# Performance work log

Hardware: AMD Instinct MI355X
Metric: run time of the kernel (lower is better)

The kernel has to match this reference:

```python
import jax, jax.numpy as jnp
import numpy as np

NEG = -1e9
EPS = 1e-5


def _layernorm(x, g, b):
    m = x.mean(-1, keepdims=True)
    v = ((x - m) ** 2).mean(-1, keepdims=True)
    return (x - m) / jnp.sqrt(v + EPS) * g + b


def _layer(h_aug, H_inc, mask_neg, W1, W1_hat, ctx1, W2, W2_hat, W3, g, b):
    # h_aug: (T, H), H_inc/mask_neg: (T, E)
    H = h_aug.shape[-1]
    scale = 1.0 / jnp.sqrt(jnp.asarray(H, h_aug.dtype))
    # Stage 1: node -> hyperedge attention
    proj_hat = h_aug @ W1_hat.T                       # (T, H)
    raw = (proj_hat * ctx1).sum(-1) * scale           # (T,)
    score = raw[:, None] + mask_neg                   # (T, E)
    alpha = jax.nn.softmax(score, axis=0) * H_inc     # (T, E)
    hyper = alpha.T @ (h_aug @ W1.T)                  # (E, H)
    # Stage 2: hyperedge -> node attention
    proj2_hat = hyper @ W2_hat.T                      # (E, H)
    score_ne = (h_aug @ W3.T) @ proj2_hat.T * scale + mask_neg  # (T, E)
    beta = jax.nn.softmax(score_ne, axis=1) * H_inc   # (T, E)
    out = beta @ (hyper @ W2.T)                       # (T, H)
    return _layernorm(out + h_aug, g, b)


def reference(node_emb, H_inc, membership, W1, W1_hat, ctx1, W2, W2_hat, W3, ln_g, ln_b, region_init):
    B, N, H = node_emb.shape
    R = region_init.shape[0]
    L = W1.shape[0]
    mask_neg = jnp.where(H_inc == 0, NEG, 0.0).astype(node_emb.dtype)
    counts = jax.ops.segment_sum(jnp.ones((N,), node_emb.dtype), membership, num_segments=R)
    safe_counts = jnp.maximum(counts, 1.0)

    def per_sample(h):  # h: (N, H)
        sums = jax.ops.segment_sum(h, membership, num_segments=R)     # (R, H)
        reg = jnp.where(counts[:, None] > 0, sums / safe_counts[:, None], 0.0)
        reg = reg + region_init
        h_aug = jnp.concatenate([h, reg], axis=0)                     # (N+R, H)
        for l in range(L):
            h_aug = _layer(h_aug, H_inc, mask_neg, W1[l], W1_hat[l], ctx1[l],
                           W2[l], W2_hat[l], W3[l], ln_g[l], ln_b[l])
        return h_aug[:N]

    return jax.vmap(per_sample)(node_emb)


def setup_inputs() -> dict:
    key = jax.random.key(0)
    ks = jax.random.split(key, 12)
    B, N, R, E, H, L = 4, 8000, 16, 1024, 128, 2
    T = N + R
    w_std = 1.0 / np.sqrt(H)
    node_emb = jax.random.normal(ks[0], (B, N, H), dtype=jnp.float32)
    H_inc = (jax.random.uniform(ks[1], (T, E)) < 0.05).astype(jnp.float32)
    membership = jax.random.randint(ks[2], (N,), 0, R, dtype=jnp.int32)
    W1 = jax.random.normal(ks[3], (L, H, H), dtype=jnp.float32) * w_std
    W1_hat = jax.random.normal(ks[4], (L, H, H), dtype=jnp.float32) * w_std
    ctx1 = jax.random.normal(ks[5], (L, H), dtype=jnp.float32) * 0.02
    W2 = jax.random.normal(ks[6], (L, H, H), dtype=jnp.float32) * w_std
    W2_hat = jax.random.normal(ks[7], (L, H, H), dtype=jnp.float32) * w_std
    W3 = jax.random.normal(ks[8], (L, H, H), dtype=jnp.float32) * w_std
    ln_g = jnp.ones((L, H), dtype=jnp.float32)
    ln_b = jnp.zeros((L, H), dtype=jnp.float32)
    region_init = jax.random.normal(ks[9], (R, H), dtype=jnp.float32) * 0.02
    return {"node_emb": node_emb, "H_inc": H_inc, "membership": membership,
            "W1": W1, "W1_hat": W1_hat, "ctx1": ctx1, "W2": W2, "W2_hat": W2_hat,
            "W3": W3, "ln_g": ln_g, "ln_b": ln_b, "region_init": region_init}
```

## Files before the change

kernel.cpp:

```cpp
#include <hip/hip_runtime.h>

#define HD 128
#define CAPE 768
#define MAXR 16
#define NB_RS 128
#define KSTR 136
#define VSTR 72
#define PSTR 72

typedef unsigned short u16;
typedef unsigned long long u64;
typedef __attribute__((ext_vector_type(8))) short bf16x8;
typedef __attribute__((ext_vector_type(4))) float f32x4;

__device__ inline float b2f(unsigned u){ return __uint_as_float(u << 16); }
__device__ inline u16 f2b(float x){
  unsigned u = __float_as_uint(x);
  return (u16)((u + 0x7fffu + ((u >> 16) & 1u)) >> 16);
}

__device__ inline float waveSum(float v){ for(int o=32;o;o>>=1) v += __shfl_down(v,o); return v; }
__device__ inline float waveMax(float v){ for(int o=32;o;o>>=1) v = fmaxf(v,__shfl_down(v,o)); return v; }

__device__ inline float blockSum128(float v, float* red){
  int j = threadIdx.x;
  float s = waveSum(v);
  __syncthreads();
  if ((j & 63) == 0) red[j >> 6] = s;
  __syncthreads();
  return red[0] + red[1];
}
__device__ inline float blockMax128(float v, float* red){
  int j = threadIdx.x;
  float s = waveMax(v);
  __syncthreads();
  if ((j & 63) == 0) red[j >> 6] = s;
  __syncthreads();
  return fmaxf(red[0], red[1]);
}

__global__ void k_count(const int* __restrict__ memb, int N, int* __restrict__ counts){
  __shared__ int h[64];
  int tid = threadIdx.x;
  if (tid < 64) h[tid] = 0;
  __syncthreads();
  for (int t = blockIdx.x*blockDim.x + tid; t < N; t += gridDim.x*blockDim.x)
    atomicAdd(&h[memb[t]], 1);
  __syncthreads();
  if (tid < 64){ int v = h[tid]; if (v) atomicAdd(&counts[tid], v); }
}

__global__ __launch_bounds__(128) void k_regsum_fast(const float* __restrict__ node,
                        const int* __restrict__ memb, int N, int R,
                        float* __restrict__ partials){
  int b = blockIdx.y, j = threadIdx.x, blk = blockIdx.x;
  int nb = gridDim.x;
  int per = (N + nb - 1) / nb;
  int t0 = blk * per;
  int t1 = t0 + per; if (t1 > N) t1 = N;
  float acc[MAXR];
  #pragma unroll
  for (int i = 0; i < MAXR; ++i) acc[i] = 0.f;
  const float* base = node + (long)b*N*HD + j;
  for (int t = t0; t < t1; ++t){
    float v = base[(long)t*HD];
    int r = memb[t];
    #pragma unroll
    for (int i = 0; i < MAXR; ++i) acc[i] += (i == r) ? v : 0.f;
  }
  float* dst = partials + ((long)(b*nb + blk)*R)*HD + j;
  #pragma unroll
  for (int i = 0; i < MAXR; ++i)
    if (i < R) dst[(long)i*HD] = acc[i];
}

__global__ void k_regsum_lds(const float* __restrict__ node, const int* __restrict__ memb,
                             int N, int R, float* __restrict__ partials, int nb){
  extern __shared__ float acc[];
  int b = blockIdx.y, j = threadIdx.x;
  for (int r = 0; r < R; ++r) acc[r*HD + j] = 0.f;
  int per = (N + gridDim.x - 1) / gridDim.x;
  int t0 = blockIdx.x * per;
  int t1 = t0 + per; if (t1 > N) t1 = N;
  for (int t = t0; t < t1; ++t){
    int r = memb[t];
    acc[r*HD + j] += node[((long)b*N + t)*HD + j];
  }
  for (int r = 0; r < R; ++r)
    atomicAdd(&partials[((long)(b*nb)*R + r)*HD + j], acc[r*HD + j]);
}

__global__ void k_regfin(const float* __restrict__ partials, int nb, int redN,
                         const int* __restrict__ counts,
                         const float* __restrict__ rinit, float* __restrict__ h_aug,
                         int N, int R, int T, int B){
  int i = blockIdx.x*blockDim.x + threadIdx.x;
  if (i >= B*R*HD) return;
  int j = i % HD; int r = (i/HD) % R; int b = i/(HD*R);
  float s = 0.f;
  for (int blk = 0; blk < redN; ++blk)
    s += partials[((long)(b*nb + blk)*R + r)*HD + j];
  int c = counts[r];
  float v = (c > 0) ? s / (float)c : 0.f;
  v += rinit[r*HD + j];
  h_aug[((long)b*T + N + r)*HD + j] = v;
}

__global__ __launch_bounds__(128) void k_copyraw(const float* __restrict__ node,
                      const float* __restrict__ v, float* __restrict__ h_aug,
                      float* __restrict__ raw, int N, int T, float scale){
  int t = blockIdx.x, b = blockIdx.y, j = threadIdx.x;
  __shared__ float red[2];
  long rowb = (long)b*T + t;
  float x;
  if (t < N){ x = node[((long)b*N + t)*HD + j]; h_aug[rowb*HD + j] = x; }
  else      { x = h_aug[rowb*HD + j]; }
  float s = blockSum128(x * v[j], red);
  if (j == 0) raw[rowb] = s * scale;
}

__global__ __launch_bounds__(256) void k_maskbuild(const float* __restrict__ Hinc, int E, int MW,
                        u64* __restrict__ maskw){
  int t = blockIdx.x;
  int wv = threadIdx.x >> 6, lane = threadIdx.x & 63;
  const float* hrow = Hinc + (long)t*E;
  for (int w = wv; w < MW; w += 4){
    int e = w*64 + lane;
    bool f = (e < E) && (hrow[e] != 0.f);
    u64 mk = __ballot(f);
    if (lane == 0) maskw[(long)t*MW + w] = mk;
  }
}

__global__ __launch_bounds__(256) void k_colbuild2(const u64* __restrict__ maskw, int T, int MW,
                           u16* __restrict__ colidx, int* __restrict__ colcnt){
  int e = blockIdx.x;
  int w = e >> 6, bit = e & 63;
  int j = threadIdx.x;
  int lane = j & 63, wv = j >> 6;
  __shared__ int wsum[4];
  int c = 0;
  for (int base = 0; base < T; base += 256){
    int t = base + j;
    bool f = (t < T) && ((maskw[(long)t*MW + w] >> bit) & 1ull);
    u64 mk = __ballot(f);
    if (lane == 0) wsum[wv] = __popcll(mk);
    __syncthreads();
    int pre = 0;
    #pragma unroll
    for (int k = 0; k < 4; ++k) pre += (k < wv) ? wsum[k] : 0;
    int tot = wsum[0] + wsum[1] + wsum[2] + wsum[3];
    if (f){
      int pos = c + pre + (int)__popcll(mk & ((1ull << lane) - 1ull));
      if (pos < CAPE) colidx[(long)e*CAPE + pos] = (u16)t;
    }
    c += tot;
    __syncthreads();
  }
  if (j == 0) colcnt[e] = (c < CAPE) ? c : CAPE;
}

__global__ void k_ctxv(const float* __restrict__ ctx1, const float* __restrict__ W1h,
                       float* __restrict__ v){
  int l = blockIdx.x, k = threadIdx.x;
  float a = 0.f;
  for (int j = 0; j < HD; ++j) a += ctx1[l*HD + j] * W1h[((long)l*HD + j)*HD + k];
  v[l*HD + k] = a;
}

__global__ void k_mm128(const float* __restrict__ W2h, const float* __restrict__ W3,
                        float* __restrict__ MqT){
  int n = blockIdx.x, l = blockIdx.y, k = threadIdx.x;
  const float* A = W2h + (long)l*HD*HD;
  const float* Bm = W3 + (long)l*HD*HD;
  float s = 0.f;
  for (int j = 0; j < HD; ++j) s += A[(long)j*HD + n] * Bm[(long)j*HD + k];
  MqT[((long)l*HD + n)*HD + k] = s;
}

__global__ __launch_bounds__(256) void k_gemmM(const float* __restrict__ A,
                       const float* __restrict__ Wa, const float* __restrict__ Wb,
                       u16* __restrict__ Cb16, float* __restrict__ Cf32, int M, int zbase){
  int isB = ((blockIdx.y + zbase) == 0) ? 1 : 0;
  const float* W = isB ? Wa : Wb;
  __shared__ __align__(16) u16 Ws[128][KSTR];
  __shared__ __align__(16) u16 As[64][KSTR];
  int tid = threadIdx.x;
  int row0 = blockIdx.x * 64;
  for (int i = tid; i < 128*128; i += 256){
    int r = i >> 7, c = i & 127;
    Ws[r][c] = f2b(W[(long)r*HD + c]);
  }
  for (int i = tid; i < 64*128; i += 256){
    int r = i >> 7, c = i & 127;
    int gr = row0 + r;
    As[r][c] = (gr < M) ? f2b(A[(long)gr*HD + c]) : (u16)0;
  }
  __syncthreads();

  int wave = tid >> 6, lane = tid & 63;
  int wr0 = wave * 16;
  int frow = lane & 15;
  int koff = (lane >> 4) * 8;
  f32x4 acc[8];
  #pragma unroll
  for (int f = 0; f < 8; ++f) acc[f] = (f32x4){0.f,0.f,0.f,0.f};

  #pragma unroll
  for (int ks = 0; ks < 4; ++ks){
    int kc = ks*32 + koff;
    bf16x8 av = *(const bf16x8*)&As[wr0 + frow][kc];
    #pragma unroll
    for (int f = 0; f < 8; ++f){
      bf16x8 bv = *(const bf16x8*)&Ws[f*16 + frow][kc];
      acc[f] = __builtin_amdgcn_mfma_f32_16x16x32_bf16(av, bv, acc[f], 0, 0, 0);
    }
  }

  int orow = wr0 + (lane >> 4) * 4;
  #pragma unroll
  for (int f = 0; f < 8; ++f){
    int col = f*16 + frow;
    #pragma unroll
    for (int i = 0; i < 4; ++i){
      int gr = row0 + orow + i;
      if (gr < M){
        if (isB) Cb16[(long)gr*HD + col] = f2b(acc[f][i]);
        else     Cf32[(long)gr*HD + col] = acc[f][i];
      }
    }
  }
}

__global__ __launch_bounds__(256) void k_gemmW2T(const float* __restrict__ W2,
                       const u16* __restrict__ hyb, u16* __restrict__ hw2t, int E){
  int b = blockIdx.y;
  int e0 = blockIdx.x * 64;
  __shared__ __align__(16) u16 As[128][KSTR];
  __shared__ __align__(16) u16 Bs[64][KSTR];
  int tid = threadIdx.x;
  for (int i = tid; i < 128*128; i += 256){
    int r = i >> 7, c = i & 127;
    As[r][c] = f2b(W2[(long)r*HD + c]);
  }
  {
    int er = tid >> 2, q = (tid & 3)*32;
    if (e0 + er < E){
      const uint4* src = (const uint4*)(hyb + ((long)b*E + e0 + er)*HD + q);
      uint4 w0 = src[0], w1 = src[1], w2 = src[2], w3 = src[3];
      *(uint4*)&Bs[er][q]    = w0;
      *(uint4*)&Bs[er][q+8]  = w1;
      *(uint4*)&Bs[er][q+16] = w2;
      *(uint4*)&Bs[er][q+24] = w3;
    } else {
      uint4 z = {0,0,0,0};
      *(uint4*)&Bs[er][q] = z; *(uint4*)&Bs[er][q+8] = z;
      *(uint4*)&Bs[er][q+16] = z; *(uint4*)&Bs[er][q+24] = z;
    }
  }
  __syncthreads();
  int wv = tid >> 6, lane = tid & 63;
  int lc = lane & 15, lg = lane >> 4;
  f32x4 acc[2][4];
  #pragma unroll
  for (int mt=0;mt<2;++mt)
    #pragma unroll
    for (int nf=0;nf<4;++nf) acc[mt][nf] = (f32x4){0.f,0.f,0.f,0.f};
  #pragma unroll
  for (int mt=0;mt<2;++mt){
    int hr = wv*32 + mt*16 + lc;
    #pragma unroll
    for (int ks=0;ks<4;++ks){
      bf16x8 av = *(const bf16x8*)&As[hr][ks*32 + lg*8];
      #pragma unroll
      for (int nf=0;nf<4;++nf){
        bf16x8 bv = *(const bf16x8*)&Bs[nf*16+lc][ks*32 + lg*8];
        acc[mt][nf] = __builtin_amdgcn_mfma_f32_16x16x32_bf16(av, bv, acc[mt][nf], 0,0,0);
      }
    }
  }
  #pragma unroll
  for (int mt=0;mt<2;++mt){
    #pragma unroll
    for (int nf=0;nf<4;++nf){
      #pragma unroll
      for (int i=0;i<4;++i){
        int h = wv*32 + mt*16 + lg*4 + i;
        int e = e0 + nf*16 + lc;
        if (e < E) hw2t[((long)b*HD + h)*E + e] = f2b(acc[mt][nf][i]);
      }
    }
  }
}

__global__ __launch_bounds__(128) void k_edge(int swz, const float* __restrict__ raw,
                      const u16* __restrict__ proj1b,
                      const int* __restrict__ colcnt, const u16* __restrict__ colidx,
                      u16* __restrict__ hyb, int T, int E){
  int bi = blockIdx.x;
  int b, e;
  if (swz){ int x = bi & 7; b = x >> 1; e = ((bi >> 3) << 1) | (x & 1); }
  else    { b = bi / E; e = bi - b*E; }
  int j = threadIdx.x;
  __shared__ float red[2];
  __shared__ float wls[CAPE];
  __shared__ int   tls[CAPE];
  int c = colcnt[e]; if (c > CAPE) c = CAPE;
  const u16* ci = colidx + (long)e*CAPE;
  const float* rawb = raw + (long)b*T;
  long orow = ((long)b*E + e)*HD + j;
  if (c <= 0){ hyb[orow] = 0; return; }
  float lm = -1e30f;
  for (int i = j; i < c; i += 128){
    int t = ci[i];
    float v = rawb[t];
    tls[i] = t;
    wls[i] = v;
    lm = fmaxf(lm, v);
  }
  float m = blockMax128(lm, red);
  float lz = 0.f;
  for (int i = j; i < c; i += 128){
    float w = __expf(wls[i] - m);
    wls[i] = w;
    lz += w;
  }
  float Z = blockSum128(lz, red);
  float invZ = 1.f / Z;
  const u16* pb = proj1b + (long)b*T*HD + j;
  float a0=0.f,a1=0.f,a2=0.f,a3=0.f;
  int i = 0;
  for (; i + 4 <= c; i += 4){
    a0 += wls[i]   * b2f(pb[(long)tls[i]  *HD]);
    a1 += wls[i+1] * b2f(pb[(long)tls[i+1]*HD]);
    a2 += wls[i+2] * b2f(pb[(long)tls[i+2]*HD]);
    a3 += wls[i+3] * b2f(pb[(long)tls[i+3]*HD]);
  }
  for (; i < c; ++i) a0 += wls[i] * b2f(pb[(long)tls[i]*HD]);
  hyb[orow] = f2b(((a0+a1)+(a2+a3)) * invZ);
}

__global__ __launch_bounds__(256) void k_flash(
      const float* __restrict__ qt, const u16* __restrict__ hyb, const u16* __restrict__ hw2t,
      const u64* __restrict__ maskw,
      const float* __restrict__ lng, const float* __restrict__ lnb,
      const float* __restrict__ vnext, float* __restrict__ rawnext, int writeRaw,
      float* __restrict__ h_aug, float* __restrict__ out,
      int T, int E, int N, int writeOut, float scale){
  int b = blockIdx.y;
  int t0 = blockIdx.x * 64;
  int tid = threadIdx.x;
  int wv = tid >> 6, lane = tid & 63;
  int lc = lane & 15, lg = lane >> 4;

  __shared__ __align__(16) u16 Ks[64][KSTR];
  __shared__ __align__(16) u16 Vs[128][VSTR];
  __shared__ __align__(16) u16 Ps[4][16][PSTR];

  int qrow = t0 + wv*16 + lc;
  bf16x8 qf[4];
  if (qrow < T){
    const float* qr = qt + ((long)b*T + qrow)*HD + lg*8;
    #pragma unroll
    for (int ks = 0; ks < 4; ++ks){
      const float4* q4 = (const float4*)(qr + ks*32);
      float4 a = q4[0], cc = q4[1];
      bf16x8 v;
      v[0]=(short)f2b(a.x);  v[1]=(short)f2b(a.y);  v[2]=(short)f2b(a.z);  v[3]=(short)f2b(a.w);
      v[4]=(short)f2b(cc.x); v[5]=(short)f2b(cc.y); v[6]=(short)f2b(cc.z); v[7]=(short)f2b(cc.w);
      qf[ks] = v;
    }
  } else {
    #pragma unroll
    for (int ks = 0; ks < 4; ++ks) qf[ks] = (bf16x8){0,0,0,0,0,0,0,0};
  }

  int mrow[4];
  #pragma unroll
  for (int i=0;i<4;++i) mrow[i] = t0 + wv*16 + lg*4 + i;

  float m_i[4], l_i[4];
  #pragma unroll
  for (int i=0;i<4;++i){ m_i[i] = -1e30f; l_i[i] = 0.f; }
  f32x4 Oa[8];
  #pragma unroll
  for (int f=0;f<8;++f) Oa[f] = (f32x4){0.f,0.f,0.f,0.f};

  const u16* hyB = hyb + (long)b*E*HD;
  const u16* vtB = hw2t + (long)b*HD*E;
  int MW = (E + 63) >> 6;
  int ntile = (E + 63) / 64;

  for (int et = 0; et < ntile; ++et){
    int e0 = et*64;
    {
      int er = tid >> 2, q = (tid & 3)*32;
      if (e0 + er < E){
        const uint4* src = (const uint4*)(hyB + (long)(e0+er)*HD + q);
        uint4 w0 = src[0], w1 = src[1], w2 = src[2], w3 = src[3];
        *(uint4*)&Ks[er][q]    = w0;
        *(uint4*)&Ks[er][q+8]  = w1;
        *(uint4*)&Ks[er][q+16] = w2;
        *(uint4*)&Ks[er][q+24] = w3;
      } else {
        uint4 z = {0,0,0,0};
        *(uint4*)&Ks[er][q] = z; *(uint4*)&Ks[er][q+8] = z;
        *(uint4*)&Ks[er][q+16] = z; *(uint4*)&Ks[er][q+24] = z;
      }
    }
    {
      int h = tid >> 1, off = (tid & 1)*32;
      if (e0 + off + 31 < E){
        const uint4* src = (const uint4*)(vtB + (long)h*E + e0 + off);
        uint4 w0 = src[0], w1 = src[1], w2 = src[2], w3 = src[3];
        *(uint4*)&Vs[h][off]    = w0;
        *(uint4*)&Vs[h][off+8]  = w1;
        *(uint4*)&Vs[h][off+16] = w2;
        *(uint4*)&Vs[h][off+24] = w3;
      } else {
        for (int k = 0; k < 32; ++k){
          int e = e0 + off + k;
          Vs[h][off+k] = (e < E) ? vtB[(long)h*E + e] : (u16)0;
        }
      }
    }
    __syncthreads();

    f32x4 accS[4];
    #pragma unroll
    for (int ne=0;ne<4;++ne) accS[ne] = (f32x4){0.f,0.f,0.f,0.f};
    #pragma unroll
    for (int ks=0;ks<4;++ks){
      #pragma unroll
      for (int ne=0;ne<4;++ne){
        bf16x8 kv = *(const bf16x8*)&Ks[ne*16+lc][ks*32 + lg*8];
        accS[ne] = __builtin_amdgcn_mfma_f32_16x16x32_bf16(qf[ks], kv, accS[ne], 0,0,0);
      }
    }

    u64 mw[4];
    #pragma unroll
    for (int i=0;i<4;++i)
      mw[i] = (mrow[i] < T) ? maskw[(long)mrow[i]*MW + et] : 0ull;

    float p[4][4];
    #pragma unroll
    for (int i=0;i<4;++i){
      float sv[4];
      float mx = -1e30f;
      #pragma unroll
      for (int ne=0;ne<4;++ne){
        int bit = (int)((mw[i] >> (ne*16 + lc)) & 1ull);
        float s = bit ? accS[ne][i]*scale : -1e30f;
        sv[ne] = s;
        mx = fmaxf(mx, s);
      }
      mx = fmaxf(mx, __shfl_xor(mx,1));
      mx = fmaxf(mx, __shfl_xor(mx,2));
      mx = fmaxf(mx, __shfl_xor(mx,4));
      mx = fmaxf(mx, __shfl_xor(mx,8));
      float mn = fmaxf(m_i[i], mx);
      float corr = __expf(m_i[i] - mn);
      m_i[i] = mn;
      float ls = 0.f;
      #pragma unroll
      for (int ne=0;ne<4;++ne){
        float pv = (sv[ne] > -1e29f) ? __expf(sv[ne] - mn) : 0.f;
        p[ne][i] = pv;
        ls += pv;
      }
      ls += __shfl_xor(ls,1);
      ls += __shfl_xor(ls,2);
      ls += __shfl_xor(ls,4);
      ls += __shfl_xor(ls,8);
      l_i[i] = l_i[i]*corr + ls;
      #pragma unroll
      for (int f=0;f<8;++f) Oa[f][i] *= corr;
    }

    #pragma unroll
    for (int i=0;i<4;++i){
      #pragma unroll
      for (int ne=0;ne<4;++ne)
        Ps[wv][lg*4+i][ne*16+lc] = f2b(p[ne][i]);
    }
    #pragma unroll
    for (int ks2=0;ks2<2;++ks2){
      bf16x8 pa = *(const bf16x8*)&Ps[wv][lc][ks2*32 + lg*8];
      #pragma unroll
      for (int f=0;f<8;++f){
        bf16x8 vb = *(const bf16x8*)&Vs[f*16+lc][ks2*32 + lg*8];
        Oa[f] = __builtin_amdgcn_mfma_f32_16x16x32_bf16(pa, vb, Oa[f], 0,0,0);
      }
    }
    __syncthreads();
  }

  #pragma unroll
  for (int i=0;i<4;++i){
    int t = mrow[i];
    if (t >= T) continue;
    long rowb = (long)b*T + t;
    float inv = (l_i[i] > 0.f) ? 1.f/l_i[i] : 0.f;
    float xv[8];
    float sm = 0.f;
    #pragma unroll
    for (int f=0;f<8;++f){
      float o = Oa[f][i]*inv;
      float h = h_aug[rowb*HD + f*16+lc];
      xv[f] = o + h;
      sm += xv[f];
    }
    sm += __shfl_xor(sm,1); sm += __shfl_xor(sm,2);
    sm += __shfl_xor(sm,4); sm += __shfl_xor(sm,8);
    float mean = sm * (1.f/HD);
    float vr = 0.f;
    #pragma unroll
    for (int f=0;f<8;++f){ float d = xv[f]-mean; vr += d*d; }
    vr += __shfl_xor(vr,1); vr += __shfl_xor(vr,2);
    vr += __shfl_xor(vr,4); vr += __shfl_xor(vr,8);
    float rstd = rsqrtf(vr*(1.f/HD) + 1e-5f);
    float rsum = 0.f;
    #pragma unroll
    for (int f=0;f<8;++f){
      int col = f*16+lc;
      float y = (xv[f]-mean)*rstd*lng[col] + lnb[col];
      if (writeOut){ if (t < N) out[((long)b*N + t)*HD + col] = y; }
      else h_aug[rowb*HD + col] = y;
      rsum += y * vnext[col];
    }
    rsum += __shfl_xor(rsum,1); rsum += __shfl_xor(rsum,2);
    rsum += __shfl_xor(rsum,4); rsum += __shfl_xor(rsum,8);
    if (writeRaw && lc == 0) rawnext[rowb] = rsum * scale;
  }
}

extern "C" void kernel_launch(void* const* d_in, const int* in_sizes, int n_in,
                              void* d_out, int out_size, void* d_ws, size_t ws_size,
                              hipStream_t stream) {
  const float* node_emb = (const float*)d_in[0];
  const float* Hinc     = (const float*)d_in[1];
  const int*   memb     = (const int*)d_in[2];
  const float* W1       = (const float*)d_in[3];
  const float* W1h      = (const float*)d_in[4];
  const float* ctx1     = (const float*)d_in[5];
  const float* W2       = (const float*)d_in[6];
  const float* W2h      = (const float*)d_in[7];
  const float* W3       = (const float*)d_in[8];
  const float* lng      = (const float*)d_in[9];
  const float* lnb      = (const float*)d_in[10];
  const float* rinit    = (const float*)d_in[11];
  float* out = (float*)d_out;

  const int N  = in_sizes[2];
  const int Hd = in_sizes[3] / in_sizes[5];
  const int L  = in_sizes[5] / Hd;
  const int R  = in_sizes[11] / Hd;
  const int B  = in_sizes[0] / (N * Hd);
  const int T  = N + R;
  const int E  = in_sizes[1] / T;
  const int MW = (E + 63) / 64;
  const float scale = 1.0f / sqrtf((float)Hd);

  char* p = (char*)d_ws;
  auto carve = [&](size_t bytes){ char* r = p; p += (bytes + 255) & ~(size_t)255; return (void*)r; };
  float* h_aug  = (float*)carve((size_t)B*T*Hd*4);
  u16*   proj1b = (u16*)  carve((size_t)B*T*Hd*2);
  float* qt     = (float*)carve((size_t)B*T*Hd*4);
  u16*   hyb    = (u16*)  carve((size_t)B*E*Hd*2);
  u16*   hw2t   = (u16*)  carve((size_t)B*Hd*E*2);
  float* MqT    = (float*)carve((size_t)L*Hd*Hd*4);
  float* rawb   = (float*)carve((size_t)B*T*4);
  float* vbuf   = (float*)carve((size_t)L*Hd*4);
  u64*   maskw  = (u64*)  carve((size_t)T*MW*8);
  int* counts   = (int*)carve((size_t)R*4);
  int* col_cnt  = (int*)carve((size_t)E*4);
  u16* col_idx  = (u16*)carve((size_t)E*CAPE*2);

  float* partials = qt;

  hipMemsetAsync(counts, 0, (size_t)R*4, stream);

  k_count<<<32, 256, 0, stream>>>(memb, N, counts);

  int redN;
  if (R <= MAXR){
    k_regsum_fast<<<dim3(NB_RS, B), 128, 0, stream>>>(node_emb, memb, N, R, partials);
    redN = NB_RS;
  } else {
    hipMemsetAsync(partials, 0, (size_t)B*R*Hd*4, stream);
    k_regsum_lds<<<dim3(16, B), Hd, (size_t)R*Hd*4, stream>>>(node_emb, memb, N, R, partials, NB_RS);
    redN = 1;
  }
  int tot = B*R*Hd;
  k_regfin<<<(tot+255)/256, 256, 0, stream>>>(partials, NB_RS, redN, counts, rinit, h_aug, N, R, T, B);

  k_maskbuild<<<T, 256, 0, stream>>>(Hinc, E, MW, maskw);
  k_colbuild2<<<E, 256, 0, stream>>>(maskw, T, MW, col_idx, col_cnt);

  k_ctxv<<<L, Hd, 0, stream>>>(ctx1, W1h, vbuf);
  k_mm128<<<dim3(Hd, L), Hd, 0, stream>>>(W2h, W3, MqT);
  k_copyraw<<<dim3(T, B), 128, 0, stream>>>(node_emb, vbuf, h_aug, rawb, N, T, scale);

  int MT = B*T;
  int gTm = (MT + 63)/64;
  int gTf = (T + 63)/64;
  int gEt = (E + 63)/64;
  int swzE = (B == 4 && (E & 1) == 0) ? 1 : 0;
  for (int l = 0; l < L; ++l){
    size_t wo = (size_t)l*Hd*Hd;
    k_gemmM<<<dim3(gTm, 2), 256, 0, stream>>>(h_aug, W1 + wo, MqT + wo, proj1b, qt, MT, 0);
    k_edge<<<B*E, 128, 0, stream>>>(swzE, rawb, proj1b, col_cnt, col_idx, hyb, T, E);
    k_gemmW2T<<<dim3(gEt, B), 256, 0, stream>>>(W2 + wo, hyb, hw2t, E);
    int writeRaw = (l < L-1) ? 1 : 0;
    const float* vnext = vbuf + (size_t)((l+1 < L) ? (l+1) : l)*Hd;
    k_flash<<<dim3(gTf, B), 256, 0, stream>>>(qt, hyb, hw2t, maskw,
                                    lng + wo/Hd, lnb + wo/Hd,
                                    vnext, rawb, writeRaw,
                                    h_aug, out, T, E, N, (l == L-1) ? 1 : 0, scale);
  }
}
```

Before: 434.0 us.

## Register-prefetch K/V tiles and keep P in registers via transposed QK MFMA

The flash-style stage-2 kernel now prefetches the next hyperedge K/V tile into registers while the current tile is computed, replacing the load-then-sync pattern. The QK^T MFMA operands are swapped so each lane holds scores for one query row, which turns the per-row softmax reductions into two cross-lane shuffles and lets the probabilities be packed straight into MFMA A operands with v_cvt_pk_bf16_f32. This drops the Ps shared-memory round trip. The V tile is stored in shared memory with a permuted column layout that matches the new register order of P, and s_setprio is raised around the MFMA blocks. In exchange, register pressure rises from the prefetch registers and the permuted indexing is error-prone.

```diff
diff --git a/kernel.cpp b/kernel.cpp
--- a/kernel.cpp
+++ b/kernel.cpp
@@ -6,12 +6,12 @@
 #define NB_RS 128
 #define KSTR 136
 #define VSTR 72
-#define PSTR 72
 
 typedef unsigned short u16;
 typedef unsigned long long u64;
 typedef __attribute__((ext_vector_type(8))) short bf16x8;
 typedef __attribute__((ext_vector_type(4))) float f32x4;
+typedef __attribute__((ext_vector_type(4))) unsigned u32x4;
 
 __device__ inline float b2f(unsigned u){ return __uint_as_float(u << 16); }
 __device__ inline u16 f2b(float x){
@@ -355,7 +355,6 @@
 
   __shared__ __align__(16) u16 Ks[64][KSTR];
   __shared__ __align__(16) u16 Vs[128][VSTR];
-  __shared__ __align__(16) u16 Ps[4][16][PSTR];
 
   int qrow = t0 + wv*16 + lc;
   bf16x8 qf[4];
@@ -375,13 +374,7 @@
     for (int ks = 0; ks < 4; ++ks) qf[ks] = (bf16x8){0,0,0,0,0,0,0,0};
   }
 
-  int mrow[4];
-  #pragma unroll
-  for (int i=0;i<4;++i) mrow[i] = t0 + wv*16 + lg*4 + i;
-
-  float m_i[4], l_i[4];
-  #pragma unroll
-  for (int i=0;i<4;++i){ m_i[i] = -1e30f; l_i[i] = 0.f; }
+  float m_s = -1e30f, l_s = 0.f;
   f32x4 Oa[8];
   #pragma unroll
   for (int f=0;f<8;++f) Oa[f] = (f32x4){0.f,0.f,0.f,0.f};
@@ -391,117 +384,166 @@
   int MW = (E + 63) >> 6;
   int ntile = (E + 63) / 64;
 
+  int kr = tid >> 2, kq = (tid & 3)*32;
+  int vh = tid >> 1, vo = (tid & 1)*32;
+
+  uint4 kreg0, kreg1, kreg2, kreg3, vreg0, vreg1, vreg2, vreg3;
+  const uint4 zz = make_uint4(0u,0u,0u,0u);
+
+  {
+    int e0 = 0;
+    if (e0 + kr < E){
+      const uint4* s = (const uint4*)(hyB + (long)(e0+kr)*HD + kq);
+      kreg0=s[0]; kreg1=s[1]; kreg2=s[2]; kreg3=s[3];
+    } else { kreg0=zz; kreg1=zz; kreg2=zz; kreg3=zz; }
+    if (e0 + vo + 31 < E){
+      const uint4* s = (const uint4*)(vtB + (long)vh*E + e0 + vo);
+      vreg0=s[0]; vreg1=s[1]; vreg2=s[2]; vreg3=s[3];
+    } else {
+      union { uint4 v[4]; u16 s[32]; } u;
+      #pragma unroll
+      for (int k=0;k<32;++k){ int e=e0+vo+k; u.s[k] = (e<E)? vtB[(long)vh*E+e] : (u16)0; }
+      vreg0=u.v[0]; vreg1=u.v[1]; vreg2=u.v[2]; vreg3=u.v[3];
+    }
+  }
+
   for (int et = 0; et < ntile; ++et){
-    int e0 = et*64;
+    *(uint4*)&Ks[kr][kq]    = kreg0;
+    *(uint4*)&Ks[kr][kq+8]  = kreg1;
+    *(uint4*)&Ks[kr][kq+16] = kreg2;
+    *(uint4*)&Ks[kr][kq+24] = kreg3;
     {
-      int er = tid >> 2, q = (tid & 3)*32;
-      if (e0 + er < E){
-        const uint4* src = (const uint4*)(hyB + (long)(e0+er)*HD + q);
-        uint4 w0 = src[0], w1 = src[1], w2 = src[2], w3 = src[3];
-        *(uint4*)&Ks[er][q]    = w0;
-        *(uint4*)&Ks[er][q+8]  = w1;
-        *(uint4*)&Ks[er][q+16] = w2;
-        *(uint4*)&Ks[er][q+24] = w3;
+      int eb0 = vo;        int ne0 = eb0>>4; int ka0 = (ne0>>1)*32 + ((eb0>>2)&3)*8 + (ne0&1)*4;
+      int eb1 = vo + 8;    int ne1 = eb1>>4; int ka1 = (ne1>>1)*32 + ((eb1>>2)&3)*8 + (ne1&1)*4;
+      int eb2 = vo + 16;   int ne2 = eb2>>4; int ka2 = (ne2>>1)*32 + ((eb2>>2)&3)*8 + (ne2&1)*4;
+      int eb3 = vo + 24;   int ne3 = eb3>>4; int ka3 = (ne3>>1)*32 + ((eb3>>2)&3)*8 + (ne3&1)*4;
+      *(uint2*)&Vs[vh][ka0]   = make_uint2(vreg0.x, vreg0.y);
+      *(uint2*)&Vs[vh][ka0+8] = make_uint2(vreg0.z, vreg0.w);
+      *(uint2*)&Vs[vh][ka1]   = make_uint2(vreg1.x, vreg1.y);
+      *(uint2*)&Vs[vh][ka1+8] = make_uint2(vreg1.z, vreg1.w);
+      *(uint2*)&Vs[vh][ka2]   = make_uint2(vreg2.x, vreg2.y);
+      *(uint2*)&Vs[vh][ka2+8] = make_uint2(vreg2.z, vreg2.w);
+      *(uint2*)&Vs[vh][ka3]   = make_uint2(vreg3.x, vreg3.y);
+      *(uint2*)&Vs[vh][ka3+8] = make_uint2(vreg3.z, vreg3.w);
+    }
+    __syncthreads();
+    if (et + 1 < ntile){
+      int e0 = (et+1)*64;
+      if (e0 + kr < E){
+        const uint4* s = (const uint4*)(hyB + (long)(e0+kr)*HD + kq);
+        kreg0=s[0]; kreg1=s[1]; kreg2=s[2]; kreg3=s[3];
+      } else { kreg0=zz; kreg1=zz; kreg2=zz; kreg3=zz; }
+      if (e0 + vo + 31 < E){
+        const uint4* s = (const uint4*)(vtB + (long)vh*E + e0 + vo);
+        vreg0=s[0]; vreg1=s[1]; vreg2=s[2]; vreg3=s[3];
       } else {
-        uint4 z = {0,0,0,0};
-        *(uint4*)&Ks[er][q] = z; *(uint4*)&Ks[er][q+8] = z;
-        *(uint4*)&Ks[er][q+16] = z; *(uint4*)&Ks[er][q+24] = z;
-      }
-    }
-    {
-      int h = tid >> 1, off = (tid & 1)*32;
-      if (e0 + off + 31 < E){
-        const uint4* src = (const uint4*)(vtB + (long)h*E + e0 + off);
-        uint4 w0 = src[0], w1 = src[1], w2 = src[2], w3 = src[3];
-        *(uint4*)&Vs[h][off]    = w0;
-        *(uint4*)&Vs[h][off+8]  = w1;
-        *(uint4*)&Vs[h][off+16] = w2;
-        *(uint4*)&Vs[h][off+24] = w3;
-      } else {
-        for (int k = 0; k < 32; ++k){
-          int e = e0 + off + k;
-          Vs[h][off+k] = (e < E) ? vtB[(long)h*E + e] : (u16)0;
-        }
-      }
-    }
-    __syncthreads();
+        union { uint4 v[4]; u16 s[32]; } u;
+        #pragma unroll
+        for (int k=0;k<32;++k){ int e=e0+vo+k; u.s[k] = (e<E)? vtB[(long)vh*E+e] : (u16)0; }
+        vreg0=u.v[0]; vreg1=u.v[1]; vreg2=u.v[2]; vreg3=u.v[3];
+      }
+    }
+
+    u64 mw = (qrow < T) ? maskw[(long)qrow*MW + et] : 0ull;
 
     f32x4 accS[4];
     #pragma unroll
     for (int ne=0;ne<4;++ne) accS[ne] = (f32x4){0.f,0.f,0.f,0.f};
+    __builtin_amdgcn_s_setprio(1);
     #pragma unroll
     for (int ks=0;ks<4;++ks){
       #pragma unroll
       for (int ne=0;ne<4;++ne){
         bf16x8 kv = *(const bf16x8*)&Ks[ne*16+lc][ks*32 + lg*8];
-        accS[ne] = __builtin_amdgcn_mfma_f32_16x16x32_bf16(qf[ks], kv, accS[ne], 0,0,0);
-      }
-    }
-
-    u64 mw[4];
-    #pragma unroll
-    for (int i=0;i<4;++i)
-      mw[i] = (mrow[i] < T) ? maskw[(long)mrow[i]*MW + et] : 0ull;
+        accS[ne] = __builtin_amdgcn_mfma_f32_16x16x32_bf16(kv, qf[ks], accS[ne], 0,0,0);
+      }
+    }
+    __builtin_amdgcn_s_setprio(0);
+
+    unsigned lo = (unsigned)mw, hi = (unsigned)(mw >> 32);
+    unsigned nib[4];
+    nib[0] = (lo >> (lg*4)) & 0xFu;
+    nib[1] = (lo >> (16 + lg*4)) & 0xFu;
+    nib[2] = (hi >> (lg*4)) & 0xFu;
+    nib[3] = (hi >> (16 + lg*4)) & 0xFu;
 
     float p[4][4];
-    #pragma unroll
-    for (int i=0;i<4;++i){
-      float sv[4];
-      float mx = -1e30f;
-      #pragma unroll
-      for (int ne=0;ne<4;++ne){
-        int bit = (int)((mw[i] >> (ne*16 + lc)) & 1ull);
-        float s = bit ? accS[ne][i]*scale : -1e30f;
-        sv[ne] = s;
+    float mx = -1e30f;
+    #pragma unroll
+    for (int ne=0;ne<4;++ne){
+      #pragma unroll
+      for (int r=0;r<4;++r){
+        float s = ((nib[ne] >> r) & 1u) ? accS[ne][r]*scale : -1e30f;
+        p[ne][r] = s;
         mx = fmaxf(mx, s);
       }
-      mx = fmaxf(mx, __shfl_xor(mx,1));
-      mx = fmaxf(mx, __shfl_xor(mx,2));
-      mx = fmaxf(mx, __shfl_xor(mx,4));
-      mx = fmaxf(mx, __shfl_xor(mx,8));
-      float mn = fmaxf(m_i[i], mx);
-      float corr = __expf(m_i[i] - mn);
-      m_i[i] = mn;
-      float ls = 0.f;
-      #pragma unroll
-      for (int ne=0;ne<4;++ne){
-        float pv = (sv[ne] > -1e29f) ? __expf(sv[ne] - mn) : 0.f;
-        p[ne][i] = pv;
+    }
+    mx = fmaxf(mx, __shfl_xor(mx, 16));
+    mx = fmaxf(mx, __shfl_xor(mx, 32));
+    float mn = fmaxf(m_s, mx);
+    float corr = __expf(m_s - mn);
+    m_s = mn;
+    float ls = 0.f;
+    #pragma unroll
+    for (int ne=0;ne<4;++ne){
+      #pragma unroll
+      for (int r=0;r<4;++r){
+        float pv = __expf(p[ne][r] - mn);
+        p[ne][r] = pv;
         ls += pv;
       }
-      ls += __shfl_xor(ls,1);
-      ls += __shfl_xor(ls,2);
-      ls += __shfl_xor(ls,4);
-      ls += __shfl_xor(ls,8);
-      l_i[i] = l_i[i]*corr + ls;
-      #pragma unroll
-      for (int f=0;f<8;++f) Oa[f][i] *= corr;
-    }
-
-    #pragma unroll
-    for (int i=0;i<4;++i){
-      #pragma unroll
-      for (int ne=0;ne<4;++ne)
-        Ps[wv][lg*4+i][ne*16+lc] = f2b(p[ne][i]);
-    }
-    #pragma unroll
-    for (int ks2=0;ks2<2;++ks2){
-      bf16x8 pa = *(const bf16x8*)&Ps[wv][lc][ks2*32 + lg*8];
+    }
+    ls += __shfl_xor(ls, 16);
+    ls += __shfl_xor(ls, 32);
+    l_s = l_s*corr + ls;
+
+    float corrO[4];
+    #pragma unroll
+    for (int i=0;i<4;++i) corrO[i] = __shfl(corr, lg*4 + i, 16);
+    #pragma unroll
+    for (int f=0;f<8;++f){
+      #pragma unroll
+      for (int i=0;i<4;++i) Oa[f][i] *= corrO[i];
+    }
+
+    unsigned pk00, pk01, pk10, pk11, pk20, pk21, pk30, pk31;
+    asm("v_cvt_pk_bf16_f32 %0, %1, %2" : "=v"(pk00) : "v"(p[0][0]), "v"(p[0][1]));
+    asm("v_cvt_pk_bf16_f32 %0, %1, %2" : "=v"(pk01) : "v"(p[0][2]), "v"(p[0][3]));
+    asm("v_cvt_pk_bf16_f32 %0, %1, %2" : "=v"(pk10) : "v"(p[1][0]), "v"(p[1][1]));
+    asm("v_cvt_pk_bf16_f32 %0, %1, %2" : "=v"(pk11) : "v"(p[1][2]), "v"(p[1][3]));
+    asm("v_cvt_pk_bf16_f32 %0, %1, %2" : "=v"(pk20) : "v"(p[2][0]), "v"(p[2][1]));
+    asm("v_cvt_pk_bf16_f32 %0, %1, %2" : "=v"(pk21) : "v"(p[2][2]), "v"(p[2][3]));
+    asm("v_cvt_pk_bf16_f32 %0, %1, %2" : "=v"(pk30) : "v"(p[3][0]), "v"(p[3][1]));
+    asm("v_cvt_pk_bf16_f32 %0, %1, %2" : "=v"(pk31) : "v"(p[3][2]), "v"(p[3][3]));
+
+    __builtin_amdgcn_s_setprio(1);
+    {
+      u32x4 w0v = { pk00, pk01, pk10, pk11 };
+      bf16x8 pa0 = __builtin_bit_cast(bf16x8, w0v);
       #pragma unroll
       for (int f=0;f<8;++f){
-        bf16x8 vb = *(const bf16x8*)&Vs[f*16+lc][ks2*32 + lg*8];
-        Oa[f] = __builtin_amdgcn_mfma_f32_16x16x32_bf16(pa, vb, Oa[f], 0,0,0);
-      }
-    }
+        bf16x8 vb = *(const bf16x8*)&Vs[f*16+lc][lg*8];
+        Oa[f] = __builtin_amdgcn_mfma_f32_16x16x32_bf16(pa0, vb, Oa[f], 0,0,0);
+      }
+      u32x4 w1v = { pk20, pk21, pk30, pk31 };
+      bf16x8 pa1 = __builtin_bit_cast(bf16x8, w1v);
+      #pragma unroll
+      for (int f=0;f<8;++f){
+        bf16x8 vb = *(const bf16x8*)&Vs[f*16+lc][32 + lg*8];
+        Oa[f] = __builtin_amdgcn_mfma_f32_16x16x32_bf16(pa1, vb, Oa[f], 0,0,0);
+      }
+    }
+    __builtin_amdgcn_s_setprio(0);
     __syncthreads();
   }
 
+  float invl = (l_s > 0.f) ? 1.f/l_s : 0.f;
   #pragma unroll
   for (int i=0;i<4;++i){
-    int t = mrow[i];
+    int t = t0 + wv*16 + lg*4 + i;
     if (t >= T) continue;
     long rowb = (long)b*T + t;
-    float inv = (l_i[i] > 0.f) ? 1.f/l_i[i] : 0.f;
+    float inv = __shfl(invl, lg*4 + i, 16);
     float xv[8];
     float sm = 0.f;
     #pragma unroll
```

Result: faster. 405.8 us (-6.5%).
